# Kernel tuning notes

Measured on AMD Instinct MI355X. Metric: run time of the kernel, lower is better.

The kernel has to match this reference:

```python
import jax, jax.numpy as jnp
import numpy as np

N_SRC = 200000
N_TGT = 40000
NNZ = 280000
D_IN = 256
D_OUT = 256
LN_EPS = 1e-5


def setup_inputs() -> dict:
    key = jax.random.key(0)
    ks = jax.random.split(key, 6)
    x = jax.random.normal(ks[0], (N_SRC, D_IN), dtype=jnp.float32)
    rows = jax.random.randint(ks[1], (NNZ,), 0, N_TGT, dtype=jnp.int32)
    cols = jax.random.randint(ks[2], (NNZ,), 0, N_SRC, dtype=jnp.int32)
    vals = jax.random.uniform(ks[3], (NNZ,), dtype=jnp.float32)
    # Linear(in_dim, out_dim) params (PyTorch-style init scale)
    W = jax.random.normal(ks[4], (D_IN, D_OUT), dtype=jnp.float32) / np.sqrt(D_IN)
    b = jnp.zeros((D_OUT,), dtype=jnp.float32)
    # LayerNorm(out_dim) params
    gamma = jnp.ones((D_OUT,), dtype=jnp.float32)
    beta = jnp.zeros((D_OUT,), dtype=jnp.float32)
    return {"x": x, "rows": rows, "cols": cols, "vals": vals,
            "W": W, "b": b, "gamma": gamma, "beta": beta,
            "num_targets": N_TGT}


def reference(x, rows, cols, vals, W, b, gamma, beta, num_targets):
    # SpMM: mapped[t, :] = sum_{e: rows[e]==t} vals[e] * x[cols[e], :]
    contrib = x[cols] * vals[:, None]                      # [nnz, d_in]
    mapped = jax.ops.segment_sum(contrib, rows, num_segments=num_targets)  # [n_tgt, d_in]
    # Linear
    h = mapped @ W + b                                     # [n_tgt, d_out]
    # LayerNorm
    mu = jnp.mean(h, axis=-1, keepdims=True)
    var = jnp.mean(jnp.square(h - mu), axis=-1, keepdims=True)
    normed = (h - mu) * jax.lax.rsqrt(var + LN_EPS) * gamma + beta
    # GELU (exact erf form, matches torch nn.GELU default)
    return jax.nn.gelu(normed, approximate=False)
```

## Files before the change

### kernel.cpp

```cpp
#include <hip/hip_runtime.h>
#include <math.h>

#define D 256
#define TM 32
#define KC 16
#define LN_EPS 1e-5f
#define SCAN_CHUNK 1024

__global__ __launch_bounds__(256) void hist_kernel(
    const int* __restrict__ rows, int* __restrict__ cnt, int nnz)
{
    const int e = blockIdx.x * 256 + threadIdx.x;
    if (e < nnz) atomicAdd(&cnt[rows[e]], 1);
}

__global__ __launch_bounds__(256) void scan1_kernel(
    const int* __restrict__ cnt, int* __restrict__ row_ptr,
    int* __restrict__ partials, int n)
{
    const int tid = threadIdx.x;
    const int base = blockIdx.x * SCAN_CHUNK + tid * 4;
    int v[4];
#pragma unroll
    for (int q = 0; q < 4; q++) {
        const int i = base + q;
        v[q] = (i < n) ? cnt[i] : 0;
    }
    const int tsum = v[0] + v[1] + v[2] + v[3];

    const int lane = tid & 63;
    int s = tsum;
#pragma unroll
    for (int off = 1; off < 64; off <<= 1) {
        const int t = __shfl_up(s, off);
        if (lane >= off) s += t;
    }
    __shared__ int wtot[4];
    if (lane == 63) wtot[tid >> 6] = s;
    __syncthreads();
    const int w = tid >> 6;
    int woff = 0;
#pragma unroll
    for (int u = 0; u < 4; u++) if (u < w) woff += wtot[u];

    int run = woff + s - tsum;
#pragma unroll
    for (int q = 0; q < 4; q++) {
        const int i = base + q;
        if (i < n) row_ptr[i] = run;
        run += v[q];
    }
    if (tid == 255) partials[blockIdx.x] = woff + s;
}

__global__ __launch_bounds__(64) void scan2_kernel(int* __restrict__ partials, int nb)
{
    const int t = threadIdx.x;
    const int v = (t < nb) ? partials[t] : 0;
    int s = v;
#pragma unroll
    for (int off = 1; off < 64; off <<= 1) {
        const int u = __shfl_up(s, off);
        if (t >= off) s += u;
    }
    if (t < nb) partials[t] = s - v;
}

__global__ __launch_bounds__(256) void scan3_kernel(
    int* __restrict__ row_ptr, int* __restrict__ cursor,
    const int* __restrict__ partials, int n, int nnz)
{
    const int tid = threadIdx.x;
    const int base = blockIdx.x * SCAN_CHUNK + tid * 4;
    const int add = partials[blockIdx.x];
#pragma unroll
    for (int q = 0; q < 4; q++) {
        const int i = base + q;
        if (i < n) {
            const int rp = row_ptr[i] + add;
            row_ptr[i] = rp;
            cursor[i]  = rp;
        }
    }
    if (blockIdx.x == 0 && tid == 0) row_ptr[n] = nnz;
}

__global__ __launch_bounds__(256) void reorder_kernel(
    const int* __restrict__ rows, const int* __restrict__ cols,
    const float* __restrict__ vals, int* __restrict__ cursor,
    int* __restrict__ scol, float* __restrict__ sval, int nnz)
{
    const int e = blockIdx.x * 256 + threadIdx.x;
    if (e < nnz) {
        const int r = rows[e];
        const int pos = atomicAdd(&cursor[r], 1);
        scol[pos] = cols[e];
        sval[pos] = vals[e];
    }
}

__global__ __launch_bounds__(256) void fused_spmm_gemm_kernel(
    const float* __restrict__ x, const int* __restrict__ row_ptr,
    const int* __restrict__ scol, const float* __restrict__ sval,
    const float* __restrict__ Wm, const float* __restrict__ bias,
    const float* __restrict__ gamma, const float* __restrict__ beta,
    float* __restrict__ out)
{
    __shared__ float As[TM][D];
    __shared__ float Bs[KC][D];

    const int tid  = threadIdx.x;
    const int wv   = tid >> 6;
    const int lane = tid & 63;
    const int r0   = blockIdx.x * TM;

    const int rbase = r0 + wv * 8;
    int rp = 0;
    if (lane < 9) rp = row_ptr[rbase + lane];

    for (int rr = 0; rr < 8; rr++) {
        const int beg = __shfl(rp, rr);
        const int end = __shfl(rp, rr + 1);

        float4 a0 = make_float4(0.f, 0.f, 0.f, 0.f);
        float4 a1 = a0, a2 = a0, a3 = a0;

        for (int cb = beg; cb < end; cb += 64) {
            const int cnt = min(64, end - cb);
            int   cidx = 0;
            float cval = 0.f;
            if (lane < cnt) {
                cidx = scol[cb + lane];
                cval = sval[cb + lane];
            }
            int j = 0;
            for (; j + 4 <= cnt; j += 4) {
                const int   c0 = __shfl(cidx, j);
                const int   c1 = __shfl(cidx, j + 1);
                const int   c2 = __shfl(cidx, j + 2);
                const int   c3 = __shfl(cidx, j + 3);
                const float v0 = __shfl(cval, j);
                const float v1 = __shfl(cval, j + 1);
                const float v2 = __shfl(cval, j + 2);
                const float v3 = __shfl(cval, j + 3);
                const float4 x0 = *(const float4*)(x + (size_t)c0 * D + 4 * lane);
                const float4 x1 = *(const float4*)(x + (size_t)c1 * D + 4 * lane);
                const float4 x2 = *(const float4*)(x + (size_t)c2 * D + 4 * lane);
                const float4 x3 = *(const float4*)(x + (size_t)c3 * D + 4 * lane);
                a0.x = fmaf(v0, x0.x, a0.x); a0.y = fmaf(v0, x0.y, a0.y);
                a0.z = fmaf(v0, x0.z, a0.z); a0.w = fmaf(v0, x0.w, a0.w);
                a1.x = fmaf(v1, x1.x, a1.x); a1.y = fmaf(v1, x1.y, a1.y);
                a1.z = fmaf(v1, x1.z, a1.z); a1.w = fmaf(v1, x1.w, a1.w);
                a2.x = fmaf(v2, x2.x, a2.x); a2.y = fmaf(v2, x2.y, a2.y);
                a2.z = fmaf(v2, x2.z, a2.z); a2.w = fmaf(v2, x2.w, a2.w);
                a3.x = fmaf(v3, x3.x, a3.x); a3.y = fmaf(v3, x3.y, a3.y);
                a3.z = fmaf(v3, x3.z, a3.z); a3.w = fmaf(v3, x3.w, a3.w);
            }
            for (; j < cnt; j++) {
                const int   c0 = __shfl(cidx, j);
                const float v0 = __shfl(cval, j);
                const float4 x0 = *(const float4*)(x + (size_t)c0 * D + 4 * lane);
                a0.x = fmaf(v0, x0.x, a0.x); a0.y = fmaf(v0, x0.y, a0.y);
                a0.z = fmaf(v0, x0.z, a0.z); a0.w = fmaf(v0, x0.w, a0.w);
            }
        }
        const float4 s = make_float4(a0.x + a1.x + a2.x + a3.x,
                                     a0.y + a1.y + a2.y + a3.y,
                                     a0.z + a1.z + a2.z + a3.z,
                                     a0.w + a1.w + a2.w + a3.w);
        *(float4*)&As[wv * 8 + rr][4 * lane] = s;
    }
    __syncthreads();

    const int tr = tid >> 5;
    const int tc = tid & 31;

    float acc[4][8];
#pragma unroll
    for (int i = 0; i < 4; i++)
#pragma unroll
        for (int j = 0; j < 8; j++) acc[i][j] = 0.f;

    for (int k0 = 0; k0 < D; k0 += KC) {
#pragma unroll
        for (int q = 0; q < 4; q++) {
            const int idx = q * 256 + tid;
            const int kk = idx >> 6;
            const int c4 = (idx & 63) * 4;
            *(float4*)&Bs[kk][c4] = *(const float4*)(Wm + (size_t)(k0 + kk) * D + c4);
        }
        __syncthreads();

#pragma unroll
        for (int q = 0; q < 4; q++) {
            float4 a4[4];
#pragma unroll
            for (int i = 0; i < 4; i++)
                a4[i] = *(const float4*)&As[tr * 4 + i][k0 + q * 4];
#pragma unroll
            for (int kk = 0; kk < 4; kk++) {
                const float4 b0 = *(const float4*)&Bs[q * 4 + kk][4 * tc];
                const float4 b1 = *(const float4*)&Bs[q * 4 + kk][128 + 4 * tc];
#pragma unroll
                for (int i = 0; i < 4; i++) {
                    const float ai = (kk == 0) ? a4[i].x :
                                     (kk == 1) ? a4[i].y :
                                     (kk == 2) ? a4[i].z : a4[i].w;
                    acc[i][0] = fmaf(ai, b0.x, acc[i][0]);
                    acc[i][1] = fmaf(ai, b0.y, acc[i][1]);
                    acc[i][2] = fmaf(ai, b0.z, acc[i][2]);
                    acc[i][3] = fmaf(ai, b0.w, acc[i][3]);
                    acc[i][4] = fmaf(ai, b1.x, acc[i][4]);
                    acc[i][5] = fmaf(ai, b1.y, acc[i][5]);
                    acc[i][6] = fmaf(ai, b1.z, acc[i][6]);
                    acc[i][7] = fmaf(ai, b1.w, acc[i][7]);
                }
            }
        }
        __syncthreads();
    }

    float gm[8], bt[8], bs[8];
#pragma unroll
    for (int j = 0; j < 8; j++) {
        const int c = (j < 4) ? (4 * tc + j) : (128 + 4 * tc + (j - 4));
        gm[j] = gamma[c]; bt[j] = beta[c]; bs[j] = bias[c];
    }

#pragma unroll
    for (int i = 0; i < 4; i++) {
        float s = 0.f, ss = 0.f;
#pragma unroll
        for (int j = 0; j < 8; j++) {
            const float h = acc[i][j] + bs[j];
            acc[i][j] = h;
            s += h; ss += h * h;
        }
#pragma unroll
        for (int off = 16; off > 0; off >>= 1) {
            s  += __shfl_xor(s,  off);
            ss += __shfl_xor(ss, off);
        }
        const float mean = s * (1.f / D);
        const float var  = ss * (1.f / D) - mean * mean;
        const float rstd = rsqrtf(var + LN_EPS);

        const int row = r0 + tr * 4 + i;
        float y[8];
#pragma unroll
        for (int j = 0; j < 8; j++) {
            const float v = (acc[i][j] - mean) * rstd * gm[j] + bt[j];
            y[j] = 0.5f * v * (1.f + erff(v * 0.70710678118654752f));
        }
        float* op = out + (size_t)row * D;
        *(float4*)(op + 4 * tc)       = make_float4(y[0], y[1], y[2], y[3]);
        *(float4*)(op + 128 + 4 * tc) = make_float4(y[4], y[5], y[6], y[7]);
    }
}

extern "C" void kernel_launch(void* const* d_in, const int* in_sizes, int n_in,
                              void* d_out, int out_size, void* d_ws, size_t ws_size,
                              hipStream_t stream) {
    const float* x     = (const float*)d_in[0];
    const int*   rows  = (const int*)d_in[1];
    const int*   cols  = (const int*)d_in[2];
    const float* vals  = (const float*)d_in[3];
    const float* Wm    = (const float*)d_in[4];
    const float* bias  = (const float*)d_in[5];
    const float* gamma = (const float*)d_in[6];
    const float* beta  = (const float*)d_in[7];
    float* out = (float*)d_out;

    const int nnz   = in_sizes[1];
    const int n_tgt = out_size / D;

    int* cnt      = (int*)d_ws;
    int* row_ptr  = cnt + n_tgt;
    int* cursor   = row_ptr + n_tgt + 1;
    int* partials = cursor + n_tgt;
    int* scol     = partials + 64;
    float* sval   = (float*)(scol + nnz);

    hipMemsetAsync(cnt, 0, (size_t)n_tgt * sizeof(int), stream);

    const int eblocks = (nnz + 255) / 256;
    hist_kernel<<<eblocks, 256, 0, stream>>>(rows, cnt, nnz);

    const int sblocks = (n_tgt + SCAN_CHUNK - 1) / SCAN_CHUNK;
    scan1_kernel<<<sblocks, 256, 0, stream>>>(cnt, row_ptr, partials, n_tgt);
    scan2_kernel<<<1, 64, 0, stream>>>(partials, sblocks);
    scan3_kernel<<<sblocks, 256, 0, stream>>>(row_ptr, cursor, partials, n_tgt, nnz);

    reorder_kernel<<<eblocks, 256, 0, stream>>>(rows, cols, vals, cursor,
                                                scol, sval, nnz);

    const int gblocks = n_tgt / TM;
    fused_spmm_gemm_kernel<<<gblocks, 256, 0, stream>>>(
        x, row_ptr, scol, sval, Wm, bias, gamma, beta, out);
}
```

Measured before the change: 445.7 us.

## Merge scan passes, widen gather unroll to 8, and halve GEMM K-chunk

Folds the single-block partial-sum scan into the scan3 kernel: each block redoes the 64-wide shuffle scan and keeps its own offset, which removes one kernel launch. The SpMM gather loop now loads 8 x rows per step with masked tails instead of 4 plus a scalar remainder, so more independent loads are in flight. The GEMM K-chunk drops from 16 to 8, which shrinks the W tile in shared memory but doubles the number of sync iterations. Masked lanes still issue redundant loads, and the Bs array size depends on KC, so it must shrink consistently.

```diff
diff --git a/kernel.cpp b/kernel.cpp
--- a/kernel.cpp
+++ b/kernel.cpp
@@ -3,7 +3,7 @@
 
 #define D 256
 #define TM 32
-#define KC 16
+#define KC 8
 #define LN_EPS 1e-5f
 #define SCAN_CHUNK 1024
 
@@ -53,26 +53,26 @@
     if (tid == 255) partials[blockIdx.x] = woff + s;
 }
 
-__global__ __launch_bounds__(64) void scan2_kernel(int* __restrict__ partials, int nb)
-{
-    const int t = threadIdx.x;
-    const int v = (t < nb) ? partials[t] : 0;
-    int s = v;
-#pragma unroll
-    for (int off = 1; off < 64; off <<= 1) {
-        const int u = __shfl_up(s, off);
-        if (t >= off) s += u;
-    }
-    if (t < nb) partials[t] = s - v;
-}
-
-__global__ __launch_bounds__(256) void scan3_kernel(
+__global__ __launch_bounds__(256) void scan23_kernel(
     int* __restrict__ row_ptr, int* __restrict__ cursor,
-    const int* __restrict__ partials, int n, int nnz)
+    const int* __restrict__ partials, int n, int nnz, int nb)
 {
     const int tid = threadIdx.x;
+    __shared__ int s_add;
+    if (tid < 64) {
+        const int v = (tid < nb) ? partials[tid] : 0;
+        int s = v;
+#pragma unroll
+        for (int off = 1; off < 64; off <<= 1) {
+            const int u = __shfl_up(s, off);
+            if (tid >= off) s += u;
+        }
+        if (tid == (int)blockIdx.x) s_add = s - v;
+    }
+    __syncthreads();
+    const int add = s_add;
+
     const int base = blockIdx.x * SCAN_CHUNK + tid * 4;
-    const int add = partials[blockIdx.x];
 #pragma unroll
     for (int q = 0; q < 4; q++) {
         const int i = base + q;
@@ -133,35 +133,29 @@
                 cidx = scol[cb + lane];
                 cval = sval[cb + lane];
             }
-            int j = 0;
-            for (; j + 4 <= cnt; j += 4) {
-                const int   c0 = __shfl(cidx, j);
-                const int   c1 = __shfl(cidx, j + 1);
-                const int   c2 = __shfl(cidx, j + 2);
-                const int   c3 = __shfl(cidx, j + 3);
-                const float v0 = __shfl(cval, j);
-                const float v1 = __shfl(cval, j + 1);
-                const float v2 = __shfl(cval, j + 2);
-                const float v3 = __shfl(cval, j + 3);
-                const float4 x0 = *(const float4*)(x + (size_t)c0 * D + 4 * lane);
-                const float4 x1 = *(const float4*)(x + (size_t)c1 * D + 4 * lane);
-                const float4 x2 = *(const float4*)(x + (size_t)c2 * D + 4 * lane);
-                const float4 x3 = *(const float4*)(x + (size_t)c3 * D + 4 * lane);
-                a0.x = fmaf(v0, x0.x, a0.x); a0.y = fmaf(v0, x0.y, a0.y);
-                a0.z = fmaf(v0, x0.z, a0.z); a0.w = fmaf(v0, x0.w, a0.w);
-                a1.x = fmaf(v1, x1.x, a1.x); a1.y = fmaf(v1, x1.y, a1.y);
-                a1.z = fmaf(v1, x1.z, a1.z); a1.w = fmaf(v1, x1.w, a1.w);
-                a2.x = fmaf(v2, x2.x, a2.x); a2.y = fmaf(v2, x2.y, a2.y);
-                a2.z = fmaf(v2, x2.z, a2.z); a2.w = fmaf(v2, x2.w, a2.w);
-                a3.x = fmaf(v3, x3.x, a3.x); a3.y = fmaf(v3, x3.y, a3.y);
-                a3.z = fmaf(v3, x3.z, a3.z); a3.w = fmaf(v3, x3.w, a3.w);
-            }
-            for (; j < cnt; j++) {
-                const int   c0 = __shfl(cidx, j);
-                const float v0 = __shfl(cval, j);
-                const float4 x0 = *(const float4*)(x + (size_t)c0 * D + 4 * lane);
-                a0.x = fmaf(v0, x0.x, a0.x); a0.y = fmaf(v0, x0.y, a0.y);
-                a0.z = fmaf(v0, x0.z, a0.z); a0.w = fmaf(v0, x0.w, a0.w);
+            for (int j = 0; j < cnt; j += 8) {
+                int   cc[8];
+                float vv[8];
+#pragma unroll
+                for (int u = 0; u < 8; u++) {
+                    const int idx = j + u;
+                    const int sl  = (idx < cnt) ? idx : j;
+                    cc[u] = __shfl(cidx, sl);
+                    vv[u] = (idx < cnt) ? __shfl(cval, sl) : 0.f;
+                }
+                float4 xv[8];
+#pragma unroll
+                for (int u = 0; u < 8; u++)
+                    xv[u] = *(const float4*)(x + (size_t)cc[u] * D + 4 * lane);
+#pragma unroll
+                for (int u = 0; u < 8; u++) {
+                    float4& a = (u & 3) == 0 ? a0 : (u & 3) == 1 ? a1 :
+                                (u & 3) == 2 ? a2 : a3;
+                    a.x = fmaf(vv[u], xv[u].x, a.x);
+                    a.y = fmaf(vv[u], xv[u].y, a.y);
+                    a.z = fmaf(vv[u], xv[u].z, a.z);
+                    a.w = fmaf(vv[u], xv[u].w, a.w);
+                }
             }
         }
         const float4 s = make_float4(a0.x + a1.x + a2.x + a3.x,
@@ -183,7 +177,7 @@
 
     for (int k0 = 0; k0 < D; k0 += KC) {
 #pragma unroll
-        for (int q = 0; q < 4; q++) {
+        for (int q = 0; q < 2; q++) {
             const int idx = q * 256 + tid;
             const int kk = idx >> 6;
             const int c4 = (idx & 63) * 4;
@@ -192,7 +186,7 @@
         __syncthreads();
 
 #pragma unroll
-        for (int q = 0; q < 4; q++) {
+        for (int q = 0; q < 2; q++) {
             float4 a4[4];
 #pragma unroll
             for (int i = 0; i < 4; i++)
@@ -288,8 +282,8 @@
 
     const int sblocks = (n_tgt + SCAN_CHUNK - 1) / SCAN_CHUNK;
     scan1_kernel<<<sblocks, 256, 0, stream>>>(cnt, row_ptr, partials, n_tgt);
-    scan2_kernel<<<1, 64, 0, stream>>>(partials, sblocks);
-    scan3_kernel<<<sblocks, 256, 0, stream>>>(row_ptr, cursor, partials, n_tgt, nnz);
+    scan23_kernel<<<sblocks, 256, 0, stream>>>(row_ptr, cursor, partials,
+                                               n_tgt, nnz, sblocks);
 
     reorder_kernel<<<eblocks, 256, 0, stream>>>(rows, cols, vals, cursor,
                                                 scol, sval, nnz);
```

Measured after the change: 424.2 us. -4.8%, faster.
